# Kernel optimization log

Hardware: AMD Instinct MI355X
Metric: run time of the kernel (lower is better)

## Reference

```python
import jax, jax.numpy as jnp
import numpy as np
import math

H = 16  # heads
EPS = 1e-6

def _ln(x, g, b):
    # Faithful to torch code: uses unbiased std (ddof=1) and divides by (std + eps)
    m = x.mean(-1, keepdims=True)
    var = ((x - m) ** 2).sum(-1, keepdims=True) / (x.shape[-1] - 1)
    return g * (x - m) / (jnp.sqrt(var) + EPS) + b

def setup_inputs() -> dict:
    key = jax.random.key(0)
    ks = jax.random.split(key, 24)
    B, S, D, F, N, O = 8, 1024, 1024, 4096, 6, 16
    s = 0.02
    w = lambda k, *sh: jax.random.normal(k, sh, jnp.float32) * s
    return {
        'x_1': jax.random.normal(ks[0], (B, S, D), jnp.float32),
        'Wq': w(ks[1], N, D, D), 'bq': jnp.zeros((N, D), jnp.float32),
        'Wk': w(ks[2], N, D, D), 'bk': jnp.zeros((N, D), jnp.float32),
        'Wv': w(ks[3], N, D, D), 'bv': jnp.zeros((N, D), jnp.float32),
        'Wo': w(ks[4], N, D, D), 'bo': jnp.zeros((N, D), jnp.float32),
        'ln0_g': jnp.ones((N, D), jnp.float32), 'ln0_b': jnp.zeros((N, D), jnp.float32),
        'W1': w(ks[5], N, D, F), 'b1': jnp.zeros((N, F), jnp.float32),
        'W2': w(ks[6], N, F, D), 'b2': jnp.zeros((N, D), jnp.float32),
        'ln1_g': jnp.ones((N, D), jnp.float32), 'ln1_b': jnp.zeros((N, D), jnp.float32),
        'lnF_g': jnp.ones((D,), jnp.float32), 'lnF_b': jnp.zeros((D,), jnp.float32),
        'Wfc': w(ks[7], D, O), 'bfc': jnp.zeros((O,), jnp.float32),
    }

def _forward(x, Wq, bq, Wk, bk, Wv, bv, Wo, bo, ln0_g, ln0_b,
             W1, b1, W2, b2, ln1_g, ln1_b, lnF_g, lnF_b, Wfc, bfc):
    B, S, D = x.shape
    dk = D // H
    scale = 1.0 / math.sqrt(dk)

    def layer(h, p):
        wq, bq_, wk, bk_, wv, bv_, wo, bo_, g0, c0, w1, c1, w2, c2, g1, c3 = p
        # pre-norm self-attention with residual (Resnet_0)
        y = _ln(h, g0, c0)
        q = (y @ wq + bq_).reshape(B, S, H, dk)
        k = (y @ wk + bk_).reshape(B, S, H, dk)
        v = (y @ wv + bv_).reshape(B, S, H, dk)
        scores = jnp.einsum('bqhd,bkhd->bhqk', q, k) * scale
        p_attn = jax.nn.softmax(scores, axis=-1)
        a = jnp.einsum('bhqk,bkhd->bqhd', p_attn, v).reshape(B, S, D)
        h = h + (a @ wo + bo_)
        # pre-norm FFN with residual (Resnet_1)
        y = _ln(h, g1, c3)
        h = h + (jax.nn.relu(y @ w1 + c1) @ w2 + c2)
        return h, None

    xs = (Wq, bq, Wk, bk, Wv, bv, Wo, bo, ln0_g, ln0_b, W1, b1, W2, b2, ln1_g, ln1_b)
    h, _ = jax.lax.scan(layer, x, xs)
    h = _ln(h, lnF_g, lnF_b)            # Encoder final norm
    feat = h[:, -1, :]                  # last-token pooling
    return jax.nn.softmax(feat @ Wfc + bfc, axis=-1)

def reference(x_1, Wq, bq, Wk, bk, Wv, bv, Wo, bo, ln0_g, ln0_b,
              W1, b1, W2, b2, ln1_g, ln1_b, lnF_g, lnF_b, Wfc, bfc):
    return _forward(x_1, Wq, bq, Wk, bk, Wv, bv, Wo, bo, ln0_g, ln0_b,
                    W1, b1, W2, b2, ln1_g, ln1_b, lnF_g, lnF_b, Wfc, bfc)
```

## Files before the change

kernel.cpp:

```cpp
#include <hip/hip_runtime.h>
#include <math.h>

typedef __attribute__((ext_vector_type(8))) short short8;
typedef __attribute__((ext_vector_type(4))) float f32x4;

#define DEV static __device__ __forceinline__

DEV unsigned short f2bf(float f) {
  union { float f; unsigned u; } x; x.f = f;
  unsigned r = x.u + 0x7fffu + ((x.u >> 16) & 1u);
  return (unsigned short)(r >> 16);
}

DEV void gload_lds16(const void* gp, void* lp) {
  __builtin_amdgcn_global_load_lds(
      (const __attribute__((address_space(1))) void*)gp,
      (__attribute__((address_space(3))) void*)lp, 16, 0, 0);
}

__global__ __launch_bounds__(256) void wconv_t(const float* __restrict__ W,
                                               unsigned short* __restrict__ Wt,
                                               int K, int N) {
  __shared__ float tile[32][33];
  int n0 = blockIdx.x * 32, k0 = blockIdx.y * 32;
  int tx = threadIdx.x, ty = threadIdx.y;
  for (int i = ty; i < 32; i += 8)
    tile[i][tx] = W[(size_t)(k0 + i) * N + n0 + tx];
  __syncthreads();
  for (int i = ty; i < 32; i += 8)
    Wt[(size_t)(n0 + i) * K + k0 + tx] = f2bf(tile[tx][i]);
}

__global__ __launch_bounds__(256) void ln_kernel(const float* __restrict__ hbuf,
                                                 const float* __restrict__ g,
                                                 const float* __restrict__ be,
                                                 unsigned short* __restrict__ y) {
  int row = blockIdx.x, tid = threadIdx.x;
  const float4 xv = reinterpret_cast<const float4*>(hbuf + (size_t)row * 1024)[tid];
  __shared__ float sbuf[4], sbuf2[4];
  float s = xv.x + xv.y + xv.z + xv.w;
  for (int off = 32; off; off >>= 1) s += __shfl_down(s, off);
  if ((tid & 63) == 0) sbuf[tid >> 6] = s;
  __syncthreads();
  float mean = (sbuf[0] + sbuf[1] + sbuf[2] + sbuf[3]) * (1.0f / 1024.0f);
  float d0 = xv.x - mean, d1 = xv.y - mean, d2 = xv.z - mean, d3 = xv.w - mean;
  float ss = d0 * d0 + d1 * d1 + d2 * d2 + d3 * d3;
  for (int off = 32; off; off >>= 1) ss += __shfl_down(ss, off);
  if ((tid & 63) == 0) sbuf2[tid >> 6] = ss;
  __syncthreads();
  float var = (sbuf2[0] + sbuf2[1] + sbuf2[2] + sbuf2[3]) * (1.0f / 1023.0f);
  float rs = 1.0f / (sqrtf(var) + 1e-6f);
  const float4 gv = reinterpret_cast<const float4*>(g)[tid];
  const float4 bv = reinterpret_cast<const float4*>(be)[tid];
  ushort4 o;
  o.x = f2bf(gv.x * d0 * rs + bv.x);
  o.y = f2bf(gv.y * d1 * rs + bv.y);
  o.z = f2bf(gv.z * d2 * rs + bv.z);
  o.w = f2bf(gv.w * d3 * rs + bv.w);
  reinterpret_cast<ushort4*>(y + (size_t)row * 1024)[tid] = o;
}

template <int EPI>
__global__ __launch_bounds__(256) void gemm_bt(const unsigned short* __restrict__ A,
                                               const unsigned short* __restrict__ Bt,
                                               const float* __restrict__ bias,
                                               unsigned short* __restrict__ Cb,
                                               float* __restrict__ Cf,
                                               int M, int N, int K) {
  __shared__ unsigned short As[128 * 32];
  __shared__ unsigned short Bs[128 * 32];
  const int tid = threadIdx.x, wave = tid >> 6, lane = tid & 63;
  const int fr = lane & 15, fq = lane >> 4;
  const int nbn = N >> 7;
  const int bm = blockIdx.x / nbn, bn = blockIdx.x % nbn;
  const int m0 = bm << 7, n0 = bn << 7;
  const int wm = (wave >> 1) << 6, wn = (wave & 1) << 6;
  f32x4 acc[4][4] = {};
  int row_a[2], col_a[2];
#pragma unroll
  for (int t = 0; t < 2; ++t) {
    int o = t * 4096 + wave * 1024 + lane * 16;
    int r = o >> 6, c2 = (o >> 4) & 3;
    row_a[t] = r;
    col_a[t] = (c2 ^ ((r >> 1) & 3)) << 3;
  }
  const unsigned short* Abase = A + (size_t)m0 * K;
  const unsigned short* Bbase = Bt + (size_t)n0 * K;
  char* AsB = (char*)As;
  char* BsB = (char*)Bs;

  for (int k0 = 0; k0 < K; k0 += 32) {
#pragma unroll
    for (int t = 0; t < 2; ++t) {
      gload_lds16(Abase + (size_t)row_a[t] * K + k0 + col_a[t], AsB + t * 4096 + wave * 1024);
      gload_lds16(Bbase + (size_t)row_a[t] * K + k0 + col_a[t], BsB + t * 4096 + wave * 1024);
    }
    __syncthreads();
    short8 af[4], bfr[4];
#pragma unroll
    for (int i = 0; i < 4; ++i) {
      int r = wm + i * 16 + fr;
      af[i] = *(const short8*)(AsB + r * 64 + ((fq ^ ((r >> 1) & 3)) << 4));
    }
#pragma unroll
    for (int j = 0; j < 4; ++j) {
      int r = wn + j * 16 + fr;
      bfr[j] = *(const short8*)(BsB + r * 64 + ((fq ^ ((r >> 1) & 3)) << 4));
    }
#pragma unroll
    for (int i = 0; i < 4; ++i)
#pragma unroll
      for (int j = 0; j < 4; ++j)
        acc[i][j] = __builtin_amdgcn_mfma_f32_16x16x32_bf16(af[i], bfr[j], acc[i][j], 0, 0, 0);
    __syncthreads();
  }
#pragma unroll
  for (int j = 0; j < 4; ++j) {
    int gcol = n0 + wn + j * 16 + fr;
    float bv = bias[gcol];
#pragma unroll
    for (int i = 0; i < 4; ++i) {
      int grow = m0 + wm + i * 16 + fq * 4;
#pragma unroll
      for (int r = 0; r < 4; ++r) {
        float val = acc[i][j][r] + bv;
        if (EPI == 1) val = fmaxf(val, 0.0f);
        if (EPI == 2) {
          size_t idx = (size_t)(grow + r) * N + gcol;
          Cf[idx] += val;
        } else {
          Cb[(size_t)(grow + r) * N + gcol] = f2bf(val);
        }
      }
    }
  }
}

__global__ __launch_bounds__(256) void attn_kernel(const unsigned short* __restrict__ Q,
                                                   const unsigned short* __restrict__ Kg,
                                                   const unsigned short* __restrict__ V,
                                                   unsigned short* __restrict__ Aout) {
  const int S = 1024, HD = 1024;
  const int bh = blockIdx.x;
  const int b = bh >> 4, hh = bh & 15;
  const int q0 = blockIdx.y << 6;
  const int tid = threadIdx.x, wave = tid >> 6, lane = tid & 63;
  const int fr = lane & 15, fq = lane >> 4;

  __shared__ unsigned short Ks[64][72];
  __shared__ unsigned short Vt[64][72];
  __shared__ unsigned short Pl[4][16][72];

  const size_t base = ((size_t)b * S) * HD + hh * 64;
  short8 qf[2];
  {
    int qrow = q0 + wave * 16 + fr;
    const unsigned short* qp = Q + base + (size_t)qrow * HD + fq * 8;
    qf[0] = *(const short8*)(qp);
    qf[1] = *(const short8*)(qp + 32);
  }
  float m_r[4] = {-INFINITY, -INFINITY, -INFINITY, -INFINITY};
  float l_r[4] = {0.f, 0.f, 0.f, 0.f};
  f32x4 oa[4] = {};

  for (int kv0 = 0; kv0 < S; kv0 += 64) {
    {
      int rr = tid >> 3, seg = tid & 7;
      const unsigned short* kp = Kg + base + (size_t)(kv0 + rr) * HD + seg * 8;
      *(short8*)&Ks[rr][seg * 8] = *(const short8*)kp;
      *(short8*)&Ks[rr + 32][seg * 8] = *(const short8*)(kp + 32 * HD);
      const unsigned short* vp = V + base + (size_t)(kv0 + rr) * HD + seg * 8;
      short8 v0 = *(const short8*)vp;
      short8 v1 = *(const short8*)(vp + 32 * HD);
#pragma unroll
      for (int j = 0; j < 8; ++j) {
        Vt[seg * 8 + j][rr] = (unsigned short)v0[j];
        Vt[seg * 8 + j][rr + 32] = (unsigned short)v1[j];
      }
    }
    __syncthreads();
    f32x4 sf[4];
#pragma unroll
    for (int fn = 0; fn < 4; ++fn) {
      f32x4 z = {};
      short8 kf0 = *(const short8*)&Ks[fn * 16 + fr][fq * 8];
      short8 kf1 = *(const short8*)&Ks[fn * 16 + fr][32 + fq * 8];
      z = __builtin_amdgcn_mfma_f32_16x16x32_bf16(qf[0], kf0, z, 0, 0, 0);
      z = __builtin_amdgcn_mfma_f32_16x16x32_bf16(qf[1], kf1, z, 0, 0, 0);
      sf[fn] = z * 0.125f;
    }
    float pr[4][4];
#pragma unroll
    for (int r = 0; r < 4; ++r) {
      float mx = fmaxf(fmaxf(sf[0][r], sf[1][r]), fmaxf(sf[2][r], sf[3][r]));
#pragma unroll
      for (int off = 1; off < 16; off <<= 1) mx = fmaxf(mx, __shfl_xor(mx, off));
      float mn = fmaxf(m_r[r], mx);
      float al = __expf(m_r[r] - mn);
      float rsum = 0.f;
#pragma unroll
      for (int fn = 0; fn < 4; ++fn) {
        float p = __expf(sf[fn][r] - mn);
        pr[fn][r] = p;
        rsum += p;
      }
#pragma unroll
      for (int off = 1; off < 16; off <<= 1) rsum += __shfl_xor(rsum, off);
      l_r[r] = l_r[r] * al + rsum;
      m_r[r] = mn;
#pragma unroll
      for (int fn = 0; fn < 4; ++fn) oa[fn][r] *= al;
    }
#pragma unroll
    for (int fn = 0; fn < 4; ++fn)
#pragma unroll
      for (int r = 0; r < 4; ++r)
        Pl[wave][fq * 4 + r][fn * 16 + fr] = f2bf(pr[fn][r]);
#pragma unroll
    for (int ks = 0; ks < 2; ++ks) {
      short8 pa = *(const short8*)&Pl[wave][fr][ks * 32 + fq * 8];
#pragma unroll
      for (int fn = 0; fn < 4; ++fn) {
        short8 vf = *(const short8*)&Vt[fn * 16 + fr][ks * 32 + fq * 8];
        oa[fn] = __builtin_amdgcn_mfma_f32_16x16x32_bf16(pa, vf, oa[fn], 0, 0, 0);
      }
    }
    __syncthreads();
  }
#pragma unroll
  for (int r = 0; r < 4; ++r) {
    float inv = 1.0f / l_r[r];
    int grow = q0 + wave * 16 + fq * 4 + r;
#pragma unroll
    for (int fn = 0; fn < 4; ++fn)
      Aout[base + (size_t)grow * HD + fn * 16 + fr] = f2bf(oa[fn][r] * inv);
  }
}

__global__ __launch_bounds__(256) void head_kernel(const float* __restrict__ hbuf,
                                                   const float* __restrict__ g,
                                                   const float* __restrict__ be,
                                                   const float* __restrict__ Wfc,
                                                   const float* __restrict__ bfc,
                                                   float* __restrict__ out) {
  int b = blockIdx.x, tid = threadIdx.x;
  const float* x = hbuf + ((size_t)b * 1024 + 1023) * 1024;
  __shared__ float sbuf[4], sbuf2[4];
  __shared__ float ybuf[1024];
  __shared__ float part[16][17];
  float4 xv = reinterpret_cast<const float4*>(x)[tid];
  float s = xv.x + xv.y + xv.z + xv.w;
  for (int off = 32; off; off >>= 1) s += __shfl_down(s, off);
  if ((tid & 63) == 0) sbuf[tid >> 6] = s;
  __syncthreads();
  float mean = (sbuf[0] + sbuf[1] + sbuf[2] + sbuf[3]) * (1.0f / 1024.0f);
  float d0 = xv.x - mean, d1 = xv.y - mean, d2 = xv.z - mean, d3 = xv.w - mean;
  float ss = d0 * d0 + d1 * d1 + d2 * d2 + d3 * d3;
  for (int off = 32; off; off >>= 1) ss += __shfl_down(ss, off);
  if ((tid & 63) == 0) sbuf2[tid >> 6] = ss;
  __syncthreads();
  float var = (sbuf2[0] + sbuf2[1] + sbuf2[2] + sbuf2[3]) * (1.0f / 1023.0f);
  float rs = 1.0f / (sqrtf(var) + 1e-6f);
  const float4 gv = reinterpret_cast<const float4*>(g)[tid];
  const float4 bv = reinterpret_cast<const float4*>(be)[tid];
  float4 yv;
  yv.x = gv.x * d0 * rs + bv.x;
  yv.y = gv.y * d1 * rs + bv.y;
  yv.z = gv.z * d2 * rs + bv.z;
  yv.w = gv.w * d3 * rs + bv.w;
  reinterpret_cast<float4*>(ybuf)[tid] = yv;
  __syncthreads();
  int n = tid & 15, pg = tid >> 4;
  float acc = 0.f;
  for (int kk = 0; kk < 64; ++kk) acc += ybuf[pg * 64 + kk] * Wfc[(size_t)(pg * 64 + kk) * 16 + n];
  part[pg][n] = acc;
  __syncthreads();
  if (tid < 16) {
    float lg = bfc[tid];
    for (int p = 0; p < 16; ++p) lg += part[p][tid];
    ybuf[tid] = lg;
  }
  __syncthreads();
  if (tid == 0) {
    float mx = ybuf[0];
    for (int i = 1; i < 16; ++i) mx = fmaxf(mx, ybuf[i]);
    float se = 0.f;
    float e[16];
    for (int i = 0; i < 16; ++i) { e[i] = __expf(ybuf[i] - mx); se += e[i]; }
    float is = 1.0f / se;
    for (int i = 0; i < 16; ++i) out[b * 16 + i] = e[i] * is;
  }
}

extern "C" void kernel_launch(void* const* d_in, const int* in_sizes, int n_in,
                              void* d_out, int out_size, void* d_ws, size_t ws_size,
                              hipStream_t stream) {
  const int B = 8, S = 1024, D = 1024, F = 4096, NL = 6;
  const int M = B * S;
  const float* x1 = (const float*)d_in[0];
  const float* Wq = (const float*)d_in[1];
  const float* bq = (const float*)d_in[2];
  const float* Wk = (const float*)d_in[3];
  const float* bk = (const float*)d_in[4];
  const float* Wv = (const float*)d_in[5];
  const float* bv = (const float*)d_in[6];
  const float* Wo = (const float*)d_in[7];
  const float* bo = (const float*)d_in[8];
  const float* ln0g = (const float*)d_in[9];
  const float* ln0b = (const float*)d_in[10];
  const float* W1 = (const float*)d_in[11];
  const float* b1 = (const float*)d_in[12];
  const float* W2 = (const float*)d_in[13];
  const float* b2 = (const float*)d_in[14];
  const float* ln1g = (const float*)d_in[15];
  const float* ln1b = (const float*)d_in[16];
  const float* lnFg = (const float*)d_in[17];
  const float* lnFb = (const float*)d_in[18];
  const float* Wfc = (const float*)d_in[19];
  const float* bfc = (const float*)d_in[20];

  char* ws = (char*)d_ws;
  size_t off = 0;
  auto carve = [&](size_t bytes) {
    char* p = ws + off;
    off += (bytes + 255) & ~(size_t)255;
    return p;
  };
  float* h = (float*)carve((size_t)M * D * 4);
  unsigned short* y = (unsigned short*)carve((size_t)M * D * 2);
  unsigned short* qb = (unsigned short*)carve((size_t)M * D * 2);
  unsigned short* kb = (unsigned short*)carve((size_t)M * D * 2);
  unsigned short* vb = (unsigned short*)carve((size_t)M * D * 2);
  unsigned short* ab = (unsigned short*)carve((size_t)M * D * 2);
  unsigned short* tb = (unsigned short*)carve((size_t)M * F * 2);
  unsigned short* wtq = (unsigned short*)carve((size_t)D * D * 2);
  unsigned short* wtk = (unsigned short*)carve((size_t)D * D * 2);
  unsigned short* wtv = (unsigned short*)carve((size_t)D * D * 2);
  unsigned short* wto = (unsigned short*)carve((size_t)D * D * 2);
  unsigned short* wt1 = (unsigned short*)carve((size_t)D * F * 2);
  unsigned short* wt2 = (unsigned short*)carve((size_t)F * D * 2);

  hipMemcpyAsync(h, x1, (size_t)M * D * 4, hipMemcpyDeviceToDevice, stream);

  dim3 tblk(32, 8);
  const int gDD = (M / 128) * (D / 128);
  const int gDF = (M / 128) * (F / 128);
  for (int l = 0; l < NL; ++l) {
    wconv_t<<<dim3(D / 32, D / 32), tblk, 0, stream>>>(Wq + (size_t)l * D * D, wtq, D, D);
    wconv_t<<<dim3(D / 32, D / 32), tblk, 0, stream>>>(Wk + (size_t)l * D * D, wtk, D, D);
    wconv_t<<<dim3(D / 32, D / 32), tblk, 0, stream>>>(Wv + (size_t)l * D * D, wtv, D, D);
    wconv_t<<<dim3(D / 32, D / 32), tblk, 0, stream>>>(Wo + (size_t)l * D * D, wto, D, D);
    wconv_t<<<dim3(F / 32, D / 32), tblk, 0, stream>>>(W1 + (size_t)l * D * F, wt1, D, F);
    wconv_t<<<dim3(D / 32, F / 32), tblk, 0, stream>>>(W2 + (size_t)l * F * D, wt2, F, D);

    ln_kernel<<<M, 256, 0, stream>>>(h, ln0g + (size_t)l * D, ln0b + (size_t)l * D, y);
    gemm_bt<0><<<gDD, 256, 0, stream>>>(y, wtq, bq + (size_t)l * D, qb, nullptr, M, D, D);
    gemm_bt<0><<<gDD, 256, 0, stream>>>(y, wtk, bk + (size_t)l * D, kb, nullptr, M, D, D);
    gemm_bt<0><<<gDD, 256, 0, stream>>>(y, wtv, bv + (size_t)l * D, vb, nullptr, M, D, D);
    attn_kernel<<<dim3(B * 16, S / 64), 256, 0, stream>>>(qb, kb, vb, ab);
    gemm_bt<2><<<gDD, 256, 0, stream>>>(ab, wto, bo + (size_t)l * D, nullptr, h, M, D, D);
    ln_kernel<<<M, 256, 0, stream>>>(h, ln1g + (size_t)l * D, ln1b + (size_t)l * D, y);
    gemm_bt<1><<<gDF, 256, 0, stream>>>(y, wt1, b1 + (size_t)l * F, tb, nullptr, M, F, D);
    gemm_bt<2><<<gDD, 256, 0, stream>>>(tb, wt2, b2 + (size_t)l * D, nullptr, h, M, D, F);
  }
  head_kernel<<<B, 256, 0, stream>>>(h, lnFg, lnFb, Wfc, bfc, (float*)d_out);
}
```

Baseline: 3.558 ms.

## Fuse QKV projections, remap GEMM blocks per XCD, rework attention softmax in registers

Combines the Q, K and V weight conversion and projection into one wider GEMM writing an interleaved QKV buffer with a concatenated bias, so fewer launches run and the activation is read once. The GEMM block index is remapped so contiguous tiles land on the same XCD, and MFMA sections raise wave priority. The attention kernel now computes S transposed so each lane holds a query column, which turns the softmax reductions into two cross-lane shuffles. P is packed to bf16 in registers instead of going through LDS. The changes add layout complexity, and the XCD remap assumes the grid size divides by 8.

Result: faster. 2.919 ms (-17.9%).

```diff
diff --git a/kernel.cpp b/kernel.cpp
--- a/kernel.cpp
+++ b/kernel.cpp
@@ -1,15 +1,16 @@
 #include <hip/hip_runtime.h>
 #include <math.h>
 
+typedef unsigned short ushort;
 typedef __attribute__((ext_vector_type(8))) short short8;
 typedef __attribute__((ext_vector_type(4))) float f32x4;
 
 #define DEV static __device__ __forceinline__
 
-DEV unsigned short f2bf(float f) {
+DEV ushort f2bf(float f) {
   union { float f; unsigned u; } x; x.f = f;
   unsigned r = x.u + 0x7fffu + ((x.u >> 16) & 1u);
-  return (unsigned short)(r >> 16);
+  return (ushort)(r >> 16);
 }
 
 DEV void gload_lds16(const void* gp, void* lp) {
@@ -19,7 +20,7 @@
 }
 
 __global__ __launch_bounds__(256) void wconv_t(const float* __restrict__ W,
-                                               unsigned short* __restrict__ Wt,
+                                               ushort* __restrict__ Wt,
                                                int K, int N) {
   __shared__ float tile[32][33];
   int n0 = blockIdx.x * 32, k0 = blockIdx.y * 32;
@@ -31,10 +32,37 @@
     Wt[(size_t)(n0 + i) * K + k0 + tx] = f2bf(tile[tx][i]);
 }
 
+__global__ __launch_bounds__(256) void wconv_qkv(const float* __restrict__ Wq,
+                                                 const float* __restrict__ Wk,
+                                                 const float* __restrict__ Wv,
+                                                 ushort* __restrict__ Wt) {
+  __shared__ float tile[32][33];
+  const float* W = blockIdx.z == 0 ? Wq : (blockIdx.z == 1 ? Wk : Wv);
+  ushort* dst = Wt + (size_t)blockIdx.z * 1024 * 1024;
+  int n0 = blockIdx.x * 32, k0 = blockIdx.y * 32;
+  int tx = threadIdx.x, ty = threadIdx.y;
+  for (int i = ty; i < 32; i += 8)
+    tile[i][tx] = W[(size_t)(k0 + i) * 1024 + n0 + tx];
+  __syncthreads();
+  for (int i = ty; i < 32; i += 8)
+    dst[(size_t)(n0 + i) * 1024 + k0 + tx] = f2bf(tile[tx][i]);
+}
+
+__global__ __launch_bounds__(256) void bias_cat(const float* __restrict__ bq,
+                                                const float* __restrict__ bk,
+                                                const float* __restrict__ bv,
+                                                float* __restrict__ bcat) {
+  int i = blockIdx.x * 256 + threadIdx.x;
+  int l = i / 3072, j = i - l * 3072;
+  float v = j < 1024 ? bq[l * 1024 + j]
+                     : (j < 2048 ? bk[l * 1024 + j - 1024] : bv[l * 1024 + j - 2048]);
+  bcat[i] = v;
+}
+
 __global__ __launch_bounds__(256) void ln_kernel(const float* __restrict__ hbuf,
                                                  const float* __restrict__ g,
                                                  const float* __restrict__ be,
-                                                 unsigned short* __restrict__ y) {
+                                                 ushort* __restrict__ y) {
   int row = blockIdx.x, tid = threadIdx.x;
   const float4 xv = reinterpret_cast<const float4*>(hbuf + (size_t)row * 1024)[tid];
   __shared__ float sbuf[4], sbuf2[4];
@@ -61,18 +89,20 @@
 }
 
 template <int EPI>
-__global__ __launch_bounds__(256) void gemm_bt(const unsigned short* __restrict__ A,
-                                               const unsigned short* __restrict__ Bt,
+__global__ __launch_bounds__(256) void gemm_bt(const ushort* __restrict__ A,
+                                               const ushort* __restrict__ Bt,
                                                const float* __restrict__ bias,
-                                               unsigned short* __restrict__ Cb,
+                                               ushort* __restrict__ Cb,
                                                float* __restrict__ Cf,
                                                int M, int N, int K) {
-  __shared__ unsigned short As[128 * 32];
-  __shared__ unsigned short Bs[128 * 32];
+  __shared__ ushort As[128 * 32];
+  __shared__ ushort Bs[128 * 32];
   const int tid = threadIdx.x, wave = tid >> 6, lane = tid & 63;
   const int fr = lane & 15, fq = lane >> 4;
   const int nbn = N >> 7;
-  const int bm = blockIdx.x / nbn, bn = blockIdx.x % nbn;
+  const int cpx = gridDim.x >> 3;
+  const int sb = (blockIdx.x & 7) * cpx + (blockIdx.x >> 3);
+  const int bm = sb / nbn, bn = sb % nbn;
   const int m0 = bm << 7, n0 = bn << 7;
   const int wm = (wave >> 1) << 6, wn = (wave & 1) << 6;
   f32x4 acc[4][4] = {};
@@ -84,8 +114,8 @@
     row_a[t] = r;
     col_a[t] = (c2 ^ ((r >> 1) & 3)) << 3;
   }
-  const unsigned short* Abase = A + (size_t)m0 * K;
-  const unsigned short* Bbase = Bt + (size_t)n0 * K;
+  const ushort* Abase = A + (size_t)m0 * K;
+  const ushort* Bbase = Bt + (size_t)n0 * K;
   char* AsB = (char*)As;
   char* BsB = (char*)Bs;
 
@@ -107,11 +137,13 @@
       int r = wn + j * 16 + fr;
       bfr[j] = *(const short8*)(BsB + r * 64 + ((fq ^ ((r >> 1) & 3)) << 4));
     }
+    __builtin_amdgcn_s_setprio(1);
 #pragma unroll
     for (int i = 0; i < 4; ++i)
 #pragma unroll
       for (int j = 0; j < 4; ++j)
         acc[i][j] = __builtin_amdgcn_mfma_f32_16x16x32_bf16(af[i], bfr[j], acc[i][j], 0, 0, 0);
+    __builtin_amdgcn_s_setprio(0);
     __syncthreads();
   }
 #pragma unroll
@@ -136,104 +168,130 @@
   }
 }
 
-__global__ __launch_bounds__(256) void attn_kernel(const unsigned short* __restrict__ Q,
-                                                   const unsigned short* __restrict__ Kg,
-                                                   const unsigned short* __restrict__ V,
-                                                   unsigned short* __restrict__ Aout) {
-  const int S = 1024, HD = 1024;
+__global__ __launch_bounds__(256) void attn3(const ushort* __restrict__ qkv,
+                                             ushort* __restrict__ Aout) {
+  const int LDQ = 3072;
   const int bh = blockIdx.x;
   const int b = bh >> 4, hh = bh & 15;
   const int q0 = blockIdx.y << 6;
   const int tid = threadIdx.x, wave = tid >> 6, lane = tid & 63;
   const int fr = lane & 15, fq = lane >> 4;
 
-  __shared__ unsigned short Ks[64][72];
-  __shared__ unsigned short Vt[64][72];
-  __shared__ unsigned short Pl[4][16][72];
-
-  const size_t base = ((size_t)b * S) * HD + hh * 64;
+  __shared__ ushort Ks[64][72];
+  __shared__ ushort Vt[64][72];
+
+  const ushort* Qb = qkv + (size_t)b * 1024 * LDQ + hh * 64;
+  const ushort* Kb = Qb + 1024;
+  const ushort* Vb = Qb + 2048;
+
   short8 qf[2];
   {
-    int qrow = q0 + wave * 16 + fr;
-    const unsigned short* qp = Q + base + (size_t)qrow * HD + fq * 8;
+    const ushort* qp = Qb + (size_t)(q0 + wave * 16 + fr) * LDQ + fq * 8;
     qf[0] = *(const short8*)(qp);
     qf[1] = *(const short8*)(qp + 32);
   }
-  float m_r[4] = {-INFINITY, -INFINITY, -INFINITY, -INFINITY};
-  float l_r[4] = {0.f, 0.f, 0.f, 0.f};
+
+  float m_run = -INFINITY, l_run = 0.0f;
   f32x4 oa[4] = {};
 
-  for (int kv0 = 0; kv0 < S; kv0 += 64) {
+  const int rr = tid >> 3, seg = tid & 7;
+  for (int kv0 = 0; kv0 < 1024; kv0 += 64) {
     {
-      int rr = tid >> 3, seg = tid & 7;
-      const unsigned short* kp = Kg + base + (size_t)(kv0 + rr) * HD + seg * 8;
+      const ushort* kp = Kb + (size_t)(kv0 + rr) * LDQ + seg * 8;
       *(short8*)&Ks[rr][seg * 8] = *(const short8*)kp;
-      *(short8*)&Ks[rr + 32][seg * 8] = *(const short8*)(kp + 32 * HD);
-      const unsigned short* vp = V + base + (size_t)(kv0 + rr) * HD + seg * 8;
+      *(short8*)&Ks[rr + 32][seg * 8] = *(const short8*)(kp + 32 * LDQ);
+      const ushort* vp = Vb + (size_t)(kv0 + rr) * LDQ + seg * 8;
       short8 v0 = *(const short8*)vp;
-      short8 v1 = *(const short8*)(vp + 32 * HD);
+      short8 v1 = *(const short8*)(vp + 32 * LDQ);
 #pragma unroll
       for (int j = 0; j < 8; ++j) {
-        Vt[seg * 8 + j][rr] = (unsigned short)v0[j];
-        Vt[seg * 8 + j][rr + 32] = (unsigned short)v1[j];
+        Vt[seg * 8 + j][rr] = (ushort)v0[j];
+        Vt[seg * 8 + j][rr + 32] = (ushort)v1[j];
       }
     }
     __syncthreads();
+
     f32x4 sf[4];
+    __builtin_amdgcn_s_setprio(1);
 #pragma unroll
     for (int fn = 0; fn < 4; ++fn) {
+      int kvr = ((fn & 1) << 5) | ((fr >> 2) << 3) | ((fn >> 1) << 2) | (fr & 3);
+      short8 kf0 = *(const short8*)&Ks[kvr][fq * 8];
+      short8 kf1 = *(const short8*)&Ks[kvr][32 + fq * 8];
       f32x4 z = {};
-      short8 kf0 = *(const short8*)&Ks[fn * 16 + fr][fq * 8];
-      short8 kf1 = *(const short8*)&Ks[fn * 16 + fr][32 + fq * 8];
-      z = __builtin_amdgcn_mfma_f32_16x16x32_bf16(qf[0], kf0, z, 0, 0, 0);
-      z = __builtin_amdgcn_mfma_f32_16x16x32_bf16(qf[1], kf1, z, 0, 0, 0);
+      z = __builtin_amdgcn_mfma_f32_16x16x32_bf16(kf0, qf[0], z, 0, 0, 0);
+      z = __builtin_amdgcn_mfma_f32_16x16x32_bf16(kf1, qf[1], z, 0, 0, 0);
       sf[fn] = z * 0.125f;
     }
-    float pr[4][4];
-#pragma unroll
-    for (int r = 0; r < 4; ++r) {
-      float mx = fmaxf(fmaxf(sf[0][r], sf[1][r]), fmaxf(sf[2][r], sf[3][r]));
-#pragma unroll
-      for (int off = 1; off < 16; off <<= 1) mx = fmaxf(mx, __shfl_xor(mx, off));
-      float mn = fmaxf(m_r[r], mx);
-      float al = __expf(m_r[r] - mn);
-      float rsum = 0.f;
-#pragma unroll
-      for (int fn = 0; fn < 4; ++fn) {
-        float p = __expf(sf[fn][r] - mn);
-        pr[fn][r] = p;
-        rsum += p;
+    __builtin_amdgcn_s_setprio(0);
+
+    float mx = sf[0][0];
+#pragma unroll
+    for (int fn = 0; fn < 4; ++fn)
+#pragma unroll
+      for (int r = 0; r < 4; ++r)
+        if (fn || r) mx = fmaxf(mx, sf[fn][r]);
+    mx = fmaxf(mx, __shfl_xor(mx, 16));
+    mx = fmaxf(mx, __shfl_xor(mx, 32));
+    float mn = fmaxf(m_run, mx);
+    float al = __expf(m_run - mn);
+    m_run = mn;
+    float p[4][4];
+    float rs = 0.0f;
+#pragma unroll
+    for (int fn = 0; fn < 4; ++fn)
+#pragma unroll
+      for (int r = 0; r < 4; ++r) {
+        float e = __expf(sf[fn][r] - mn);
+        p[fn][r] = e;
+        rs += e;
       }
-#pragma unroll
-      for (int off = 1; off < 16; off <<= 1) rsum += __shfl_xor(rsum, off);
-      l_r[r] = l_r[r] * al + rsum;
-      m_r[r] = mn;
-#pragma unroll
-      for (int fn = 0; fn < 4; ++fn) oa[fn][r] *= al;
-    }
+    rs += __shfl_xor(rs, 16);
+    rs += __shfl_xor(rs, 32);
+    l_run = l_run * al + rs;
+    float alo[4];
+#pragma unroll
+    for (int r = 0; r < 4; ++r) alo[r] = __shfl(al, (fq << 2) + r);
 #pragma unroll
     for (int fn = 0; fn < 4; ++fn)
 #pragma unroll
-      for (int r = 0; r < 4; ++r)
-        Pl[wave][fq * 4 + r][fn * 16 + fr] = f2bf(pr[fn][r]);
+      for (int r = 0; r < 4; ++r) oa[fn][r] *= alo[r];
+
+    unsigned pw[4][2];
+#pragma unroll
+    for (int fn = 0; fn < 4; ++fn)
+#pragma unroll
+      for (int h2 = 0; h2 < 2; ++h2)
+        asm("v_cvt_pk_bf16_f32 %0, %1, %2"
+            : "=v"(pw[fn][h2])
+            : "v"(p[fn][2 * h2]), "v"(p[fn][2 * h2 + 1]));
+
+    __builtin_amdgcn_s_setprio(1);
 #pragma unroll
     for (int ks = 0; ks < 2; ++ks) {
-      short8 pa = *(const short8*)&Pl[wave][fr][ks * 32 + fq * 8];
+      union { unsigned w[4]; short8 s; } pu;
+      pu.w[0] = pw[ks][0]; pu.w[1] = pw[ks][1];
+      pu.w[2] = pw[ks + 2][0]; pu.w[3] = pw[ks + 2][1];
 #pragma unroll
       for (int fn = 0; fn < 4; ++fn) {
         short8 vf = *(const short8*)&Vt[fn * 16 + fr][ks * 32 + fq * 8];
-        oa[fn] = __builtin_amdgcn_mfma_f32_16x16x32_bf16(pa, vf, oa[fn], 0, 0, 0);
+        oa[fn] = __builtin_amdgcn_mfma_f32_16x16x32_bf16(pu.s, vf, oa[fn], 0, 0, 0);
       }
     }
+    __builtin_amdgcn_s_setprio(0);
     __syncthreads();
   }
+
+  float linv = 1.0f / l_run;
+  float li[4];
+#pragma unroll
+  for (int r = 0; r < 4; ++r) li[r] = __shfl(linv, (fq << 2) + r);
 #pragma unroll
   for (int r = 0; r < 4; ++r) {
-    float inv = 1.0f / l_r[r];
-    int grow = q0 + wave * 16 + fq * 4 + r;
+    size_t orow = (size_t)(b * 1024 + q0 + wave * 16 + fq * 4 + r);
 #pragma unroll
     for (int fn = 0; fn < 4; ++fn)
-      Aout[base + (size_t)grow * HD + fn * 16 + fr] = f2bf(oa[fn][r] * inv);
+      Aout[orow * 1024 + hh * 64 + fn * 16 + fr] = f2bf(oa[fn][r] * li[r]);
   }
 }
 
@@ -327,37 +385,34 @@
     return p;
   };
   float* h = (float*)carve((size_t)M * D * 4);
-  unsigned short* y = (unsigned short*)carve((size_t)M * D * 2);
-  unsigned short* qb = (unsigned short*)carve((size_t)M * D * 2);
-  unsigned short* kb = (unsigned short*)carve((size_t)M * D * 2);
-  unsigned short* vb = (unsigned short*)carve((size_t)M * D * 2);
-  unsigned short* ab = (unsigned short*)carve((size_t)M * D * 2);
-  unsigned short* tb = (unsigned short*)carve((size_t)M * F * 2);
-  unsigned short* wtq = (unsigned short*)carve((size_t)D * D * 2);
-  unsigned short* wtk = (unsigned short*)carve((size_t)D * D * 2);
-  unsigned short* wtv = (unsigned short*)carve((size_t)D * D * 2);
-  unsigned short* wto = (unsigned short*)carve((size_t)D * D * 2);
-  unsigned short* wt1 = (unsigned short*)carve((size_t)D * F * 2);
-  unsigned short* wt2 = (unsigned short*)carve((size_t)F * D * 2);
+  ushort* y = (ushort*)carve((size_t)M * D * 2);
+  ushort* qkvb = (ushort*)carve((size_t)M * 3 * D * 2);
+  ushort* ab = (ushort*)carve((size_t)M * D * 2);
+  ushort* tb = (ushort*)carve((size_t)M * F * 2);
+  ushort* wtqkv = (ushort*)carve((size_t)3 * D * D * 2);
+  ushort* wto = (ushort*)carve((size_t)D * D * 2);
+  ushort* wt1 = (ushort*)carve((size_t)D * F * 2);
+  ushort* wt2 = (ushort*)carve((size_t)F * D * 2);
+  float* bcat = (float*)carve((size_t)NL * 3 * D * 4);
 
   hipMemcpyAsync(h, x1, (size_t)M * D * 4, hipMemcpyDeviceToDevice, stream);
+  bias_cat<<<(NL * 3 * D) / 256, 256, 0, stream>>>(bq, bk, bv, bcat);
 
   dim3 tblk(32, 8);
+  const int gQKV = (M / 128) * ((3 * D) / 128);
   const int gDD = (M / 128) * (D / 128);
   const int gDF = (M / 128) * (F / 128);
   for (int l = 0; l < NL; ++l) {
-    wconv_t<<<dim3(D / 32, D / 32), tblk, 0, stream>>>(Wq + (size_t)l * D * D, wtq, D, D);
-    wconv_t<<<dim3(D / 32, D / 32), tblk, 0, stream>>>(Wk + (size_t)l * D * D, wtk, D, D);
-    wconv_t<<<dim3(D / 32, D / 32), tblk, 0, stream>>>(Wv + (size_t)l * D * D, wtv, D, D);
+    wconv_qkv<<<dim3(D / 32, D / 32, 3), tblk, 0, stream>>>(
+        Wq + (size_t)l * D * D, Wk + (size_t)l * D * D, Wv + (size_t)l * D * D, wtqkv);
     wconv_t<<<dim3(D / 32, D / 32), tblk, 0, stream>>>(Wo + (size_t)l * D * D, wto, D, D);
     wconv_t<<<dim3(F / 32, D / 32), tblk, 0, stream>>>(W1 + (size_t)l * D * F, wt1, D, F);
     wconv_t<<<dim3(D / 32, F / 32), tblk, 0, stream>>>(W2 + (size_t)l * F * D, wt2, F, D);
 
     ln_kernel<<<M, 256, 0, stream>>>(h, ln0g + (size_t)l * D, ln0b + (size_t)l * D, y);
-    gemm_bt<0><<<gDD, 256, 0, stream>>>(y, wtq, bq + (size_t)l * D, qb, nullptr, M, D, D);
-    gemm_bt<0><<<gDD, 256, 0, stream>>>(y, wtk, bk + (size_t)l * D, kb, nullptr, M, D, D);
-    gemm_bt<0><<<gDD, 256, 0, stream>>>(y, wtv, bv + (size_t)l * D, vb, nullptr, M, D, D);
-    attn_kernel<<<dim3(B * 16, S / 64), 256, 0, stream>>>(qb, kb, vb, ab);
+    gemm_bt<0><<<gQKV, 256, 0, stream>>>(y, wtqkv, bcat + (size_t)l * 3 * D, qkvb, nullptr,
+                                         M, 3 * D, D);
+    attn3<<<dim3(B * 16, S / 64), 256, 0, stream>>>(qkvb, ab);
     gemm_bt<2><<<gDD, 256, 0, stream>>>(ab, wto, bo + (size_t)l * D, nullptr, h, M, D, D);
     ln_kernel<<<M, 256, 0, stream>>>(h, ln1g + (size_t)l * D, ln1b + (size_t)l * D, y);
     gemm_bt<1><<<gDF, 256, 0, stream>>>(y, wt1, b1 + (size_t)l * F, tb, nullptr, M, F, D);
```
